# Performance work log

Measured on AMD Instinct MI355X. Metric: run time of the kernel, lower is better.

Reference implementation:

```python
import jax, jax.numpy as jnp
from jax import lax
import numpy as np

# Mamba2 config from PixelMamba.__init__
D_MODEL = 128; D_STATE = 256; D_CONV = 4; EXPAND = 4; HEADDIM = 32
D_INNER = EXPAND * D_MODEL              # 512
NHEADS = D_INNER // HEADDIM             # 16
NGROUPS = 1
D_XBC = D_INNER + 2 * NGROUPS * D_STATE # 1024 (conv channels)
D_IN_PROJ = 2 * D_INNER + 2 * NGROUPS * D_STATE + NHEADS  # 1552
CHUNK = 128                             # SSD chunk length


def setup_inputs() -> dict:
    key = jax.random.key(0)
    ks = jax.random.split(key, 10)
    Bb, C, H, W = 2, 3, 64, 64
    f32 = jnp.float32
    rn = lambda k, shape, s: jax.random.normal(k, shape, f32) * s
    return {
        "x": jax.random.normal(ks[0], (Bb, C, H, W), f32),
        "fc0_w": rn(ks[1], (3, D_MODEL), 1.0 / np.sqrt(3.0)),
        "fc0_b": rn(ks[2], (D_MODEL,), 0.01),
        "in_proj_w": rn(ks[3], (D_MODEL, D_IN_PROJ), 1.0 / np.sqrt(D_MODEL)),
        "conv_w": rn(ks[4], (D_XBC, D_CONV), 1.0 / np.sqrt(D_CONV)),
        "conv_b": rn(ks[5], (D_XBC,), 0.01),
        "dt_bias": jnp.log(jnp.expm1(jax.random.uniform(ks[6], (NHEADS,), f32, 0.001, 0.1))),
        "A_log": jnp.log(jax.random.uniform(ks[7], (NHEADS,), f32, 1.0, 16.0)),
        "D": rn(ks[8], (NHEADS,), 1.0),
        "norm_w": jnp.ones((D_INNER,), f32),
        "out_proj_w": rn(ks[9], (D_INNER, D_MODEL), 1.0 / np.sqrt(D_INNER)),
    }


def _mamba2(u, in_proj_w, conv_w, conv_b, dt_bias, A_log, D, norm_w, out_proj_w):
    # u: (B, L, d_model)
    Bb, L, _ = u.shape
    zxbcdt = u @ in_proj_w                                     # (B,L,1552)
    z = zxbcdt[..., :D_INNER]                                  # gate
    xBC = zxbcdt[..., D_INNER:D_INNER + D_XBC]
    dt = jax.nn.softplus(zxbcdt[..., -NHEADS:] + dt_bias)     # (B,L,H)

    # causal depthwise conv1d + SiLU
    xc = lax.conv_general_dilated(
        xBC.transpose(0, 2, 1), conv_w[:, None, :], (1,), [(D_CONV - 1, 0)],
        dimension_numbers=('NCH', 'OIH', 'NCH'), feature_group_count=D_XBC)
    xBC = jax.nn.silu(xc + conv_b[None, :, None]).transpose(0, 2, 1)

    xs = xBC[..., :D_INNER].reshape(Bb, L, NHEADS, HEADDIM)    # (B,L,H,P)
    Bm = xBC[..., D_INNER:D_INNER + D_STATE]                   # (B,L,N), ngroups=1
    Cm = xBC[..., D_INNER + D_STATE:]                          # (B,L,N)
    A = -jnp.exp(A_log)                                        # (H,) negative

    # ---- SSD chunked selective scan ----
    NC = L // CHUNK
    a = (dt * A).reshape(Bb, NC, CHUNK, NHEADS)                # log-decay per step (<=0)
    dt_r = dt.reshape(Bb, NC, CHUNK, NHEADS)
    x_r = xs.reshape(Bb, NC, CHUNK, NHEADS, HEADDIM)
    B_r = Bm.reshape(Bb, NC, CHUNK, D_STATE)
    C_r = Cm.reshape(Bb, NC, CHUNK, D_STATE)
    cum = jnp.cumsum(a, axis=2)                                # (B,NC,Q,H)

    # intra-chunk quadratic part: attn[t,s] = (C_t.B_s) * exp(cum_t - cum_s) * dt_s, s<=t
    mask = jnp.tril(jnp.ones((CHUNK, CHUNK), bool))
    diff = cum[:, :, :, None, :] - cum[:, :, None, :, :]       # (B,NC,t,s,H)
    decay = jnp.exp(jnp.where(mask[None, None, :, :, None], diff, -jnp.inf))
    CB = jnp.einsum('bctn,bcsn->bcts', C_r, B_r)
    attn = CB[..., None] * decay * dt_r[:, :, None, :, :]      # (B,NC,t,s,H)
    y_intra = jnp.einsum('bctsh,bcshp->bcthp', attn, x_r)

    # per-chunk end states: sum_s exp(cum_end - cum_s) dt_s x_s B_s^T
    decay_end = jnp.exp(cum[:, :, -1:, :] - cum)               # (B,NC,Q,H)
    states = jnp.einsum('bcsh,bcsn,bcshp->bchpn', decay_end * dt_r, B_r, x_r)

    # inter-chunk recurrence over NC chunks (small sequential scan)
    chunk_decay = jnp.exp(cum[:, :, -1, :])                    # (B,NC,H)
    def step(S, inp):
        cd, st = inp
        return S * cd[..., None, None] + st, S                 # emit state BEFORE chunk
    S0 = jnp.zeros((Bb, NHEADS, HEADDIM, D_STATE), u.dtype)
    _, prev = lax.scan(step, S0, (chunk_decay.transpose(1, 0, 2),
                                  states.transpose(1, 0, 2, 3, 4)))
    prev = prev.transpose(1, 0, 2, 3, 4)                       # (B,NC,H,P,N)
    y_inter = jnp.einsum('bcth,bctn,bchpn->bcthp', jnp.exp(cum), C_r, prev)

    y = (y_intra + y_inter).reshape(Bb, L, NHEADS, HEADDIM) + D[None, None, :, None] * xs
    y = y.reshape(Bb, L, D_INNER)

    # gated RMSNorm (norm_before_gate=False): norm(y * silu(z)) * w
    y = y * jax.nn.silu(z)
    y = y * lax.rsqrt(jnp.mean(y * y, axis=-1, keepdims=True) + 1e-5) * norm_w
    return y @ out_proj_w


def reference(x, fc0_w, fc0_b, in_proj_w, conv_w, conv_b, dt_bias, A_log, D, norm_w, out_proj_w):
    Bb, C, H, W = x.shape
    x1 = x.transpose(0, 2, 3, 1).reshape(Bb, -1, C)            # raster order
    x2 = x[:, :, ::-1, ::-1].transpose(0, 2, 3, 1).reshape(Bb, -1, C)  # flipped
    u = jnp.concatenate([x1, x2], axis=1) @ fc0_w + fc0_b      # (B, 2HW, 128)
    return _mamba2(u, in_proj_w, conv_w, conv_b, dt_bias, A_log, D, norm_w, out_proj_w)
```

## Files before the change

### kernel.cpp

```cpp
#include <hip/hip_runtime.h>
#include <hip/hip_bf16.h>

typedef short short8 __attribute__((ext_vector_type(8)));
typedef float f32x4 __attribute__((ext_vector_type(4)));
typedef unsigned short ushort;
typedef unsigned int uint;

#define MFMA16(a,b,c) __builtin_amdgcn_mfma_f32_16x16x32_bf16(a,b,c,0,0,0)
#define DPROJ 1552
#define LOG2E 1.44269504f

constexpr size_t OFF_M    = 0;
constexpr size_t OFF_CB_B = 0x5000;
constexpr size_t OFF_WT   = 0x8000;
constexpr size_t OFF_XT   = 0x30000;
constexpr size_t OFF_DT   = OFF_XT  + 16777216ull;
constexpr size_t OFF_BCM  = OFF_DT  + 1048576ull;
constexpr size_t OFF_CUM  = OFF_BCM + 16777216ull;
constexpr size_t OFF_CDC  = OFF_CUM + 1048576ull;
constexpr size_t OFF_CBT  = OFF_CDC + 8192ull;
constexpr size_t OFF_BT   = OFF_CBT + 4194304ull;
constexpr size_t OFF_ST   = OFF_BT  + 8388608ull;
constexpr size_t OFF_Y    = OFF_ST  + 33554432ull;

__device__ __forceinline__ float sigm(float x){ return 1.0f/(1.0f + __expf(-x)); }
__device__ __forceinline__ ushort f2bf(float f){
  union { __hip_bfloat16 h; ushort u; } c;
  c.h = __float2bfloat16(f);
  return c.u;
}
__device__ __forceinline__ float bf2f(ushort h){
  union { uint u; float f; } c; c.u = ((uint)h)<<16;
  return c.f;
}
__device__ __forceinline__ void swz2048(int p, int& bc, int& h){
  int xcd = p & 7, slot = p >> 3;
  bc = xcd*16 + (slot >> 4);
  h  = slot & 15;
}

__global__ __launch_bounds__(256) void k0m_prep(const float* __restrict__ fc0_w,
                                                const float* __restrict__ fc0_b,
                                                const float* __restrict__ W,
                                                const float* __restrict__ norm_w,
                                                const float* __restrict__ Wout,
                                                char* __restrict__ wsb){
  int d = blockIdx.x;
  ushort* WT = (ushort*)(wsb + OFF_WT);
  for (int i = threadIdx.x; i < 512; i += 256)
    WT[(size_t)d*512 + i] = f2bf(norm_w[i]*Wout[(size_t)i*128 + d]);
  if (d < 7){
    int j = d*256 + threadIdx.x;
    if (j >= DPROJ) return;
    float* Mo = (float*)(wsb + OFF_M);
    float* Co = (float*)(wsb + OFF_CB_B);
    float m0=0.f,m1=0.f,m2=0.f,cc=0.f;
    for (int dd=0; dd<128; ++dd){
      float w = W[(size_t)dd*DPROJ + j];
      m0 = fmaf(fc0_w[dd],     w, m0);
      m1 = fmaf(fc0_w[128+dd], w, m1);
      m2 = fmaf(fc0_w[256+dd], w, m2);
      cc = fmaf(fc0_b[dd],     w, cc);
    }
    Mo[j] = m0; Mo[DPROJ + j] = m1; Mo[2*DPROJ + j] = m2;
    Co[j] = cc;
  }
}

__device__ __forceinline__ void proj8(int li, const float* __restrict__ xb,
                                      const float* m0, const float* m1, const float* m2,
                                      const float* c8, float* dst){
  if (li < 0){
    #pragma unroll
    for (int j=0;j<8;++j) dst[j] = 0.f;
    return;
  }
  int hh, wv;
  if (li < 4096){ hh = li>>6; wv = li&63; }
  else { int l2 = li-4096; hh = 63-(l2>>6); wv = 63-(l2&63); }
  float x0 = xb[hh*64+wv], x1 = xb[4096+hh*64+wv], x2 = xb[8192+hh*64+wv];
  #pragma unroll
  for (int j=0;j<8;++j)
    dst[j] = fmaf(x2, m2[j], fmaf(x1, m1[j], fmaf(x0, m0[j], c8[j])));
}

__device__ __forceinline__ void conv8(const float* cb8, const float* cw0, const float* cw1,
                                      const float* cw2, const float* cw3,
                                      const float* wA, const float* wB,
                                      const float* wC, const float* wD, ushort* o){
  #pragma unroll
  for (int j=0;j<8;++j){
    float a = cb8[j];
    a = fmaf(wA[j], cw0[j], a);
    a = fmaf(wB[j], cw1[j], a);
    a = fmaf(wC[j], cw2[j], a);
    a = fmaf(wD[j], cw3[j], a);
    o[j] = f2bf(a * sigm(a));
  }
}

__global__ __launch_bounds__(256) void k12_projconv(const float* __restrict__ x,
                                                    const float* __restrict__ conv_w,
                                                    const float* __restrict__ conv_b,
                                                    char* __restrict__ wsb){
  int tid = threadIdx.x;
  int cg = tid & 127, rl = tid >> 7;
  int row0 = blockIdx.x*16 + rl*8;
  int b = row0 >> 13, l0 = row0 & 8191;
  const float* M  = (const float*)(wsb + OFF_M);
  const float* Cc = (const float*)(wsb + OFF_CB_B);
  const float* xb = x + (size_t)b*12288;
  int ch0 = cg*8, j0 = 512 + ch0;
  float m0[8],m1[8],m2[8],c8[8],cw0[8],cw1[8],cw2[8],cw3[8],cb8[8];
  #pragma unroll
  for (int j=0;j<8;++j){
    m0[j]=M[j0+j]; m1[j]=M[DPROJ+j0+j]; m2[j]=M[2*DPROJ+j0+j]; c8[j]=Cc[j0+j];
    cw0[j]=conv_w[(ch0+j)*4+0]; cw1[j]=conv_w[(ch0+j)*4+1];
    cw2[j]=conv_w[(ch0+j)*4+2]; cw3[j]=conv_w[(ch0+j)*4+3];
    cb8[j]=conv_b[ch0+j];
  }
  bool is_xs = (ch0 < 512);
  bool is_b  = (ch0 >= 512) && (ch0 < 768);
  bool pack  = is_xs || is_b;
  ushort* bcmp = (ushort*)(wsb + OFF_BCM);
  int chb = ch0 - 512;
  uint colw[8][4];
  ushort oprev[8];
  float w0[8],w1[8],w2[8],w3[8];
  ushort o[8];
  proj8(l0-3, xb, m0,m1,m2,c8, w1);
  proj8(l0-2, xb, m0,m1,m2,c8, w2);
  proj8(l0-1, xb, m0,m1,m2,c8, w3);

#define ROW_EVEN(R, WN, WA, WB, WC)                                          \
  proj8(l0+R, xb, m0,m1,m2,c8, WN);                                          \
  conv8(cb8,cw0,cw1,cw2,cw3, WA,WB,WC,WN, o);                                \
  if (pack){ _Pragma("unroll")                                               \
    for (int j=0;j<8;++j) oprev[j] = o[j]; }                                 \
  if (!is_xs) *(uint4*)(bcmp + (size_t)(row0+R)*512 + chb) = *(uint4*)o;
#define ROW_ODD(R, WN, WA, WB, WC)                                           \
  proj8(l0+R, xb, m0,m1,m2,c8, WN);                                          \
  conv8(cb8,cw0,cw1,cw2,cw3, WA,WB,WC,WN, o);                                \
  if (pack){ _Pragma("unroll")                                               \
    for (int j=0;j<8;++j) colw[j][(R)>>1] = (uint)oprev[j] | ((uint)o[j]<<16); } \
  if (!is_xs) *(uint4*)(bcmp + (size_t)(row0+R)*512 + chb) = *(uint4*)o;

  ROW_EVEN(0, w0, w1,w2,w3)
  ROW_ODD (1, w1, w2,w3,w0)
  ROW_EVEN(2, w2, w3,w0,w1)
  ROW_ODD (3, w3, w0,w1,w2)
  ROW_EVEN(4, w0, w1,w2,w3)
  ROW_ODD (5, w1, w2,w3,w0)
  ROW_EVEN(6, w2, w3,w0,w1)
  ROW_ODD (7, w3, w0,w1,w2)
#undef ROW_EVEN
#undef ROW_ODD

  int bc = row0>>7, grp = (row0&127)>>3;
  if (is_xs){
    int h = ch0>>5, p0 = ch0&31;
    ushort* dst = (ushort*)(wsb+OFF_XT) + (((size_t)(bc*16+h)*16 + grp)*32)*8;
    #pragma unroll
    for (int j=0;j<8;++j){
      uint4 v; v.x = colw[j][0]; v.y = colw[j][1]; v.z = colw[j][2]; v.w = colw[j][3];
      *(uint4*)(dst + (size_t)(p0+j)*8) = v;
    }
  } else if (is_b){
    ushort* btb = (ushort*)(wsb+OFF_BT) + (size_t)bc*32768;
    #pragma unroll
    for (int j=0;j<8;++j){
      uint4 v; v.x = colw[j][0]; v.y = colw[j][1]; v.z = colw[j][2]; v.w = colw[j][3];
      *(uint4*)(btb + (size_t)(grp*256 + chb + j)*8) = v;
    }
  }
}

__global__ __launch_bounds__(256) void k4m(const float* __restrict__ x,
                                           const float* __restrict__ dt_bias,
                                           const float* __restrict__ A_log,
                                           char* __restrict__ wsb){
  __shared__ __align__(16) char sMem[20480];
  int tid = threadIdx.x;
  int lane = tid&63, wid = tid>>6, l15 = lane&15, l4 = lane>>4;

  if (blockIdx.x < 2048){
    int bc, h; swz2048(blockIdx.x, bc, h);
    int bi = bc*16 + h;
    float* sCS = (float*)sMem;
    float* sW  = (float*)(sMem + 512);
    const ushort* xt  = (const ushort*)(wsb + OFF_XT) + (size_t)bi*4096;
    const ushort* btb = (const ushort*)(wsb + OFF_BT) + (size_t)bc*32768;
    ushort* st = (ushort*)(wsb + OFF_ST) + (size_t)bi*8192;
    float dtv = 0.f;
    if (tid < 128){
      int r = bc*128 + tid;
      int b = r >> 13, l = r & 8191;
      int hp, wv;
      if (l < 4096){ hp = l>>6; wv = l&63; }
      else { int l2 = l-4096; hp = 63-(l2>>6); wv = 63-(l2&63); }
      const float* xb = x + (size_t)b*12288;
      float x0 = xb[hp*64+wv], x1 = xb[4096+hp*64+wv], x2 = xb[8192+hp*64+wv];
      const float* M  = (const float*)(wsb + OFF_M);
      const float* Cc = (const float*)(wsb + OFF_CB_B);
      int j = 1536 + h;
      float v = Cc[j];
      v = fmaf(x0, M[j], v);
      v = fmaf(x1, M[DPROJ+j], v);
      v = fmaf(x2, M[2*DPROJ+j], v);
      float tt = v + dt_bias[h];
      dtv = (tt > 20.f) ? tt : log1pf(__expf(tt));
      ((float*)(wsb+OFF_DT))[(size_t)r*16 + h] = dtv;
      float A2 = -__expf(A_log[h]) * LOG2E;
      sCS[tid] = dtv * A2;
    }
    __syncthreads();
    for (int off=1; off<128; off<<=1){
      float sv = (tid>=off && tid<128) ? sCS[tid-off] : 0.f;
      __syncthreads();
      if (tid < 128) sCS[tid] += sv;
      __syncthreads();
    }
    if (tid < 128){
      float cv = sCS[tid];
      ((float*)(wsb + OFF_CUM))[(size_t)bi*128 + tid] = cv;
      if (tid == 127) ((float*)(wsb + OFF_CDC))[bi] = exp2f(cv);
    }
    __syncthreads();
    if (tid < 128) sW[tid] = exp2f(sCS[127] - sCS[tid]) * dtv;
    __syncthreads();
    f32x4 acc2[2][4] = {};
    #pragma unroll
    for (int ks = 0; ks < 4; ++ks){
      int grp = ks*4 + l4;
      const float* wp = sW + grp*8;
      short8 ra0 = *(const short8*)(xt + (size_t)(grp*32 + l15)*8);
      short8 ra1 = *(const short8*)(xt + (size_t)(grp*32 + 16 + l15)*8);
      short8 a0, a1;
      #pragma unroll
      for (int j=0;j<8;++j){
        a0[j] = (short)f2bf(bf2f((ushort)ra0[j]) * wp[j]);
        a1[j] = (short)f2bf(bf2f((ushort)ra1[j]) * wp[j]);
      }
      #pragma unroll
      for (int ntl = 0; ntl < 4; ++ntl){
        int n = wid*64 + ntl*16 + l15;
        short8 b = *(const short8*)(btb + (size_t)(grp*256 + n)*8);
        acc2[0][ntl] = MFMA16(a0,b,acc2[0][ntl]);
        acc2[1][ntl] = MFMA16(a1,b,acc2[1][ntl]);
      }
    }
    #pragma unroll
    for (int mt=0; mt<2; ++mt)
    #pragma unroll
    for (int ntl=0; ntl<4; ++ntl)
    #pragma unroll
    for (int r=0; r<4; ++r){
      int p = mt*16 + l4*4 + r;
      int n = wid*64 + ntl*16 + l15;
      st[(size_t)((n>>3)*32 + p)*8 + (n&7)] = f2bf(acc2[mt][ntl][r]);
    }
  } else {
    int bi = blockIdx.x - 2048;
    int sq = bi & 3; int bc = bi >> 2;
    char* sC = sMem;
    char* sB = sMem + 16384;
    const ushort* bcm = (const ushort*)(wsb + OFF_BCM);
    ushort* cbtT = (ushort*)(wsb + OFF_CBT) + (size_t)bc*16384;
    size_t rb = (size_t)bc*128;
    int s_base = sq*32;
    f32x4 acc[2][2] = {};
    for (int nt = 0; nt < 4; ++nt){
      int n0 = nt*64;
      __syncthreads();
      for (int idx = tid; idx < 1024; idx += 256){
        int t = idx>>3, c = idx&7;
        uint4 v = *(const uint4*)(bcm + (rb+t)*512 + 256 + n0 + c*8);
        *(uint4*)(sC + ((t*128 + c*16) ^ ((t&7)<<4))) = v;
      }
      {
        int idx = tid;
        int s = idx>>3, c = idx&7;
        uint4 v = *(const uint4*)(bcm + (rb+s_base+s)*512 + n0 + c*8);
        *(uint4*)(sB + ((s*128 + c*16) ^ ((s&7)<<4))) = v;
      }
      __syncthreads();
      if (wid >= sq){
        #pragma unroll
        for (int ks = 0; ks < 2; ++ks){
          int kb = ks*64 + l4*16;
          int t0 = wid*32 + l15, t1 = t0 + 16;
          short8 a0 = *(const short8*)(sC + ((t0*128 + kb) ^ ((t0&7)<<4)));
          short8 a1 = *(const short8*)(sC + ((t1*128 + kb) ^ ((t1&7)<<4)));
          short8 b0 = *(const short8*)(sB + ((l15*128 + kb) ^ ((l15&7)<<4)));
          short8 b1 = *(const short8*)(sB + (((16+l15)*128 + kb) ^ (((16+l15)&7)<<4)));
          acc[0][0] = MFMA16(a0,b0,acc[0][0]);
          acc[0][1] = MFMA16(a0,b1,acc[0][1]);
          acc[1][0] = MFMA16(a1,b0,acc[1][0]);
          acc[1][1] = MFMA16(a1,b1,acc[1][1]);
        }
      }
    }
    #pragma unroll
    for (int mt=0; mt<2; ++mt)
    #pragma unroll
    for (int st=0; st<2; ++st)
    #pragma unroll
    for (int r=0; r<4; ++r){
      int t = wid*32 + mt*16 + l4*4 + r;
      int s = s_base + st*16 + l15;
      float v = (t >= s) ? acc[mt][st][r] : 0.f;
      cbtT[(size_t)((s>>3)*128 + t)*8 + (s&7)] = f2bf(v);
    }
  }
}

__global__ __launch_bounds__(256) void k5_scan(char* __restrict__ wsb){
  int g = blockIdx.x*256 + threadIdx.x;
  int idx32 = g*2;
  int e = idx32 & 7;
  int q = idx32 >> 3;
  int p = q & 31; q >>= 5;
  int grp = q & 31; q >>= 5;
  int h = q & 15; int b = q >> 4;
  int off32 = (grp*32 + p)*4 + (e>>1);
  uint* st32 = (uint*)(wsb + OFF_ST);
  const float* cdc = (const float*)(wsb + OFF_CDC);
  float S0 = 0.f, S1 = 0.f;
  for (int c=0; c<64; ++c){
    int bi = (b*64+c)*16 + h;
    size_t idx = (size_t)bi*4096 + off32;
    uint v = st32[idx];
    float v0 = bf2f((ushort)(v & 0xFFFFu));
    float v1 = bf2f((ushort)(v >> 16));
    st32[idx] = (uint)f2bf(S0) | ((uint)f2bf(S1) << 16);
    float cd = cdc[bi];
    S0 = fmaf(S0, cd, v0);
    S1 = fmaf(S1, cd, v1);
  }
}

__global__ __launch_bounds__(256) void k4y_out(const float* __restrict__ Dp,
                                               char* __restrict__ wsb){
  int bc, h; swz2048(blockIdx.x, bc, h);
  int bi = bc*16 + h;
  __shared__ float sCum[128], sDt[128], sE[128];
  __shared__ __align__(16) char sPrev[16384];
  __shared__ __align__(16) char sXT[8192];
  const ushort* cbt = (const ushort*)(wsb + OFF_CBT) + (size_t)bc*16384;
  const char* xtg   = (const char*)(wsb + OFF_XT) + (size_t)bi*8192;
  const char* prevg = (const char*)(wsb + OFF_ST) + (size_t)bi*16384;
  const ushort* bcm = (const ushort*)(wsb + OFF_BCM);
  const float* cum  = (const float*)(wsb + OFF_CUM) + (size_t)bi*128;
  const float* dtp  = (const float*)(wsb + OFF_DT);
  ushort* Yb = (ushort*)(wsb + OFF_Y);
  size_t rb = (size_t)bc*128;
  int tid = threadIdx.x;
  #pragma unroll
  for (int i=0;i<4;++i)
    *(uint4*)(sPrev + i*4096 + tid*16) = *(const uint4*)(prevg + (size_t)i*4096 + tid*16);
  #pragma unroll
  for (int i=0;i<2;++i)
    *(uint4*)(sXT + i*4096 + tid*16) = *(const uint4*)(xtg + (size_t)i*4096 + tid*16);
  if (tid < 128){
    float cv = cum[tid];
    sCum[tid] = cv;
    sDt[tid]  = dtp[(rb+tid)*16 + h];
    sE[tid]   = exp2f(cv);
  }
  __syncthreads();
  int lane = tid&63, wid = tid>>6, l15 = lane&15, l4 = lane>>4;
  int t0 = wid*32 + l15, t1 = t0 + 16;
  float ct0 = sCum[t0], ct1 = sCum[t1];
  f32x4 acc[2][2] = {};
  #pragma unroll
  for (int ks = 0; ks < 4; ++ks){
    if (ks <= wid){
      int grp = ks*4 + l4;
      int s0 = grp*8;
      short8 ra0 = *(const short8*)(cbt + (size_t)(grp*128 + t0)*8);
      short8 ra1 = *(const short8*)(cbt + (size_t)(grp*128 + t1)*8);
      short8 a0, a1;
      #pragma unroll
      for (int j=0;j<8;++j){
        int s = s0 + j;
        float cs = sCum[s], ds = sDt[s];
        float e0 = exp2f(fminf(ct0 - cs, 0.f)) * ds;
        float e1 = exp2f(fminf(ct1 - cs, 0.f)) * ds;
        a0[j] = (short)f2bf(bf2f((ushort)ra0[j]) * e0);
        a1[j] = (short)f2bf(bf2f((ushort)ra1[j]) * e1);
      }
      short8 b0 = *(const short8*)(sXT + (grp*32 + l15)*16);
      short8 b1 = *(const short8*)(sXT + (grp*32 + 16 + l15)*16);
      acc[0][0] = MFMA16(a0,b0,acc[0][0]);
      acc[0][1] = MFMA16(a0,b1,acc[0][1]);
      acc[1][0] = MFMA16(a1,b0,acc[1][0]);
      acc[1][1] = MFMA16(a1,b1,acc[1][1]);
    }
  }
  f32x4 acc2[2][2] = {};
  #pragma unroll
  for (int ks = 0; ks < 8; ++ks){
    int koff = ks*32 + l4*8;
    int grp = ks*4 + l4;
    short8 a0 = *(const short8*)(bcm + (rb+t0)*512 + 256 + koff);
    short8 a1 = *(const short8*)(bcm + (rb+t1)*512 + 256 + koff);
    short8 b0 = *(const short8*)(sPrev + (grp*32 + l15)*16);
    short8 b1 = *(const short8*)(sPrev + (grp*32 + 16 + l15)*16);
    acc2[0][0] = MFMA16(a0,b0,acc2[0][0]);
    acc2[0][1] = MFMA16(a0,b1,acc2[0][1]);
    acc2[1][0] = MFMA16(a1,b0,acc2[1][0]);
    acc2[1][1] = MFMA16(a1,b1,acc2[1][1]);
  }
  float Dh = Dp[h];
  #pragma unroll
  for (int mt=0; mt<2; ++mt){
    int tb = wid*32 + mt*16 + l4*4;
    int tg = tb>>3, e0i = tb&7;
    #pragma unroll
    for (int nt=0; nt<2; ++nt){
      int p = nt*16 + l15;
      ushort xv[4];
      *(uint2*)xv = *(const uint2*)(sXT + ((tg*32 + p)*8 + e0i)*2);
      #pragma unroll
      for (int r=0; r<4; ++r){
        int t = tb + r;
        float yv = acc[mt][nt][r] + sE[t]*acc2[mt][nt][r] + Dh*bf2f(xv[r]);
        Yb[(rb+t)*512 + h*32 + p] = f2bf(yv);
      }
    }
  }
}

__global__ __launch_bounds__(256) void k7_final(const float* __restrict__ x,
                                                char* __restrict__ wsb,
                                                float* __restrict__ out){
  int r0 = blockIdx.x*32;
  __shared__ __align__(16) char sG[32768];
  __shared__ float sScale[32];
  const ushort* Yb = (const ushort*)(wsb + OFF_Y);
  const float* M  = (const float*)(wsb + OFF_M);
  const float* Cb = (const float*)(wsb + OFF_CB_B);
  const ushort* WT = (const ushort*)(wsb + OFF_WT);
  int tid = threadIdx.x;
  int r = tid>>3, li = tid&7;
  int row = r0 + r; int b = row>>13, l = row & 8191;
  int hh, wv;
  if (l < 4096){ hh = l>>6; wv = l&63; }
  else { int l2 = l-4096; hh = 63-(l2>>6); wv = 63-(l2&63); }
  const float* xb = x + (size_t)b*12288;
  float x0 = xb[hh*64+wv], x1 = xb[4096+hh*64+wv], x2 = xb[8192+hh*64+wv];
  float sq = 0.f;
  #pragma unroll
  for (int k = 0; k < 8; ++k){
    int i0 = li*64 + k*8;
    short8 yv = *(const short8*)(Yb + (size_t)row*512 + i0);
    ushort g8[8];
    #pragma unroll
    for (int j=0;j<8;++j){
      int i = i0 + j;
      float z = Cb[i];
      z = fmaf(x0, M[i], z);
      z = fmaf(x1, M[DPROJ+i], z);
      z = fmaf(x2, M[2*DPROJ+i], z);
      float g = bf2f((ushort)yv[j]) * z * sigm(z);
      sq = fmaf(g, g, sq);
      g8[j] = f2bf(g);
    }
    *(uint4*)(sG + ((r*1024 + i0*2) ^ ((r&7)<<4))) = *(uint4*)g8;
  }
  sq += __shfl_xor(sq, 1, 64);
  sq += __shfl_xor(sq, 2, 64);
  sq += __shfl_xor(sq, 4, 64);
  if (li == 0) sScale[r] = rsqrtf(sq*(1.f/512.f) + 1e-5f);
  __syncthreads();
  int lane = tid&63, wid = tid>>6, l15 = lane&15, l4 = lane>>4;
  f32x4 acc[2][2] = {};
  #pragma unroll
  for (int ks = 0; ks < 16; ++ks){
    int kb = ks*64 + l4*16;
    int rr0 = l15, rr1 = 16+l15;
    short8 a0 = *(const short8*)(sG + ((rr0*1024 + kb) ^ ((rr0&7)<<4)));
    short8 a1 = *(const short8*)(sG + ((rr1*1024 + kb) ^ ((rr1&7)<<4)));
    int koff = ks*32 + l4*8;
    short8 b0 = *(const short8*)(WT + (size_t)(wid*32 + l15)*512 + koff);
    short8 b1 = *(const short8*)(WT + (size_t)(wid*32 + 16 + l15)*512 + koff);
    acc[0][0] = MFMA16(a0,b0,acc[0][0]);
    acc[0][1] = MFMA16(a0,b1,acc[0][1]);
    acc[1][0] = MFMA16(a1,b0,acc[1][0]);
    acc[1][1] = MFMA16(a1,b1,acc[1][1]);
  }
  #pragma unroll
  for (int mt=0; mt<2; ++mt)
  #pragma unroll
  for (int nt=0; nt<2; ++nt)
  #pragma unroll
  for (int r4=0; r4<4; ++r4){
    int rr = mt*16 + l4*4 + r4;
    int d = wid*32 + nt*16 + l15;
    out[(size_t)(r0+rr)*128 + d] = acc[mt][nt][r4] * sScale[rr];
  }
}

extern "C" void kernel_launch(void* const* d_in, const int* in_sizes, int n_in,
                              void* d_out, int out_size, void* d_ws, size_t ws_size,
                              hipStream_t stream) {
  const float* x         = (const float*)d_in[0];
  const float* fc0_w     = (const float*)d_in[1];
  const float* fc0_b     = (const float*)d_in[2];
  const float* in_proj_w = (const float*)d_in[3];
  const float* conv_w    = (const float*)d_in[4];
  const float* conv_b    = (const float*)d_in[5];
  const float* dt_bias   = (const float*)d_in[6];
  const float* A_log     = (const float*)d_in[7];
  const float* Dp        = (const float*)d_in[8];
  const float* norm_w    = (const float*)d_in[9];
  const float* out_proj_w= (const float*)d_in[10];
  char* wsb  = (char*)d_ws;
  float* out = (float*)d_out;

  k0m_prep<<<dim3(128),  dim3(256), 0, stream>>>(fc0_w, fc0_b, in_proj_w, norm_w, out_proj_w, wsb);
  k12_projconv<<<dim3(1024), dim3(256), 0, stream>>>(x, conv_w, conv_b, wsb);
  k4m    <<<dim3(2560),  dim3(256), 0, stream>>>(x, dt_bias, A_log, wsb);
  k5_scan<<<dim3(512),   dim3(256), 0, stream>>>(wsb);
  k4y_out<<<dim3(2048),  dim3(256), 0, stream>>>(Dp, wsb);
  k7_final<<<dim3(512),  dim3(256), 0, stream>>>(x, wsb, out);
}
```

Baseline: 138.4 us.

## Rework k4m: wave-shuffle cumsum, direct-global CB GEMM, reorder block roles

The 128-element cumulative sum of dt*A is now done with wavefront shuffle-up scans plus one shared-memory fixup, replacing the barrier-heavy log-step scan. The C·B^T block branch now reads operands straight from global memory instead of staging them through swizzled LDS tiles, and the full K=256 loop runs without barriers. The CB blocks are moved to the front of the grid, and shared memory shrinks to two small float arrays, which should raise occupancy. The cost is more uncached or uncoalesced global reads of the B/C rows in the CB branch.

Result: no change. 137.8 us (median of 2 runs) (-0.4%).

```diff
diff --git a/kernel.cpp b/kernel.cpp
--- a/kernel.cpp
+++ b/kernel.cpp
@@ -179,125 +179,32 @@
                                            const float* __restrict__ dt_bias,
                                            const float* __restrict__ A_log,
                                            char* __restrict__ wsb){
-  __shared__ __align__(16) char sMem[20480];
+  __shared__ float sCS[128];
+  __shared__ float sW[128];
   int tid = threadIdx.x;
   int lane = tid&63, wid = tid>>6, l15 = lane&15, l4 = lane>>4;
 
-  if (blockIdx.x < 2048){
-    int bc, h; swz2048(blockIdx.x, bc, h);
-    int bi = bc*16 + h;
-    float* sCS = (float*)sMem;
-    float* sW  = (float*)(sMem + 512);
-    const ushort* xt  = (const ushort*)(wsb + OFF_XT) + (size_t)bi*4096;
-    const ushort* btb = (const ushort*)(wsb + OFF_BT) + (size_t)bc*32768;
-    ushort* st = (ushort*)(wsb + OFF_ST) + (size_t)bi*8192;
-    float dtv = 0.f;
-    if (tid < 128){
-      int r = bc*128 + tid;
-      int b = r >> 13, l = r & 8191;
-      int hp, wv;
-      if (l < 4096){ hp = l>>6; wv = l&63; }
-      else { int l2 = l-4096; hp = 63-(l2>>6); wv = 63-(l2&63); }
-      const float* xb = x + (size_t)b*12288;
-      float x0 = xb[hp*64+wv], x1 = xb[4096+hp*64+wv], x2 = xb[8192+hp*64+wv];
-      const float* M  = (const float*)(wsb + OFF_M);
-      const float* Cc = (const float*)(wsb + OFF_CB_B);
-      int j = 1536 + h;
-      float v = Cc[j];
-      v = fmaf(x0, M[j], v);
-      v = fmaf(x1, M[DPROJ+j], v);
-      v = fmaf(x2, M[2*DPROJ+j], v);
-      float tt = v + dt_bias[h];
-      dtv = (tt > 20.f) ? tt : log1pf(__expf(tt));
-      ((float*)(wsb+OFF_DT))[(size_t)r*16 + h] = dtv;
-      float A2 = -__expf(A_log[h]) * LOG2E;
-      sCS[tid] = dtv * A2;
-    }
-    __syncthreads();
-    for (int off=1; off<128; off<<=1){
-      float sv = (tid>=off && tid<128) ? sCS[tid-off] : 0.f;
-      __syncthreads();
-      if (tid < 128) sCS[tid] += sv;
-      __syncthreads();
-    }
-    if (tid < 128){
-      float cv = sCS[tid];
-      ((float*)(wsb + OFF_CUM))[(size_t)bi*128 + tid] = cv;
-      if (tid == 127) ((float*)(wsb + OFF_CDC))[bi] = exp2f(cv);
-    }
-    __syncthreads();
-    if (tid < 128) sW[tid] = exp2f(sCS[127] - sCS[tid]) * dtv;
-    __syncthreads();
-    f32x4 acc2[2][4] = {};
-    #pragma unroll
-    for (int ks = 0; ks < 4; ++ks){
-      int grp = ks*4 + l4;
-      const float* wp = sW + grp*8;
-      short8 ra0 = *(const short8*)(xt + (size_t)(grp*32 + l15)*8);
-      short8 ra1 = *(const short8*)(xt + (size_t)(grp*32 + 16 + l15)*8);
-      short8 a0, a1;
-      #pragma unroll
-      for (int j=0;j<8;++j){
-        a0[j] = (short)f2bf(bf2f((ushort)ra0[j]) * wp[j]);
-        a1[j] = (short)f2bf(bf2f((ushort)ra1[j]) * wp[j]);
-      }
-      #pragma unroll
-      for (int ntl = 0; ntl < 4; ++ntl){
-        int n = wid*64 + ntl*16 + l15;
-        short8 b = *(const short8*)(btb + (size_t)(grp*256 + n)*8);
-        acc2[0][ntl] = MFMA16(a0,b,acc2[0][ntl]);
-        acc2[1][ntl] = MFMA16(a1,b,acc2[1][ntl]);
-      }
-    }
-    #pragma unroll
-    for (int mt=0; mt<2; ++mt)
-    #pragma unroll
-    for (int ntl=0; ntl<4; ++ntl)
-    #pragma unroll
-    for (int r=0; r<4; ++r){
-      int p = mt*16 + l4*4 + r;
-      int n = wid*64 + ntl*16 + l15;
-      st[(size_t)((n>>3)*32 + p)*8 + (n&7)] = f2bf(acc2[mt][ntl][r]);
-    }
-  } else {
-    int bi = blockIdx.x - 2048;
-    int sq = bi & 3; int bc = bi >> 2;
-    char* sC = sMem;
-    char* sB = sMem + 16384;
+  if (blockIdx.x < 512){
+    int bi4 = blockIdx.x;
+    int sq = bi4 & 3; int bc = bi4 >> 2;
     const ushort* bcm = (const ushort*)(wsb + OFF_BCM);
     ushort* cbtT = (ushort*)(wsb + OFF_CBT) + (size_t)bc*16384;
     size_t rb = (size_t)bc*128;
     int s_base = sq*32;
     f32x4 acc[2][2] = {};
-    for (int nt = 0; nt < 4; ++nt){
-      int n0 = nt*64;
-      __syncthreads();
-      for (int idx = tid; idx < 1024; idx += 256){
-        int t = idx>>3, c = idx&7;
-        uint4 v = *(const uint4*)(bcm + (rb+t)*512 + 256 + n0 + c*8);
-        *(uint4*)(sC + ((t*128 + c*16) ^ ((t&7)<<4))) = v;
-      }
-      {
-        int idx = tid;
-        int s = idx>>3, c = idx&7;
-        uint4 v = *(const uint4*)(bcm + (rb+s_base+s)*512 + n0 + c*8);
-        *(uint4*)(sB + ((s*128 + c*16) ^ ((s&7)<<4))) = v;
-      }
-      __syncthreads();
-      if (wid >= sq){
-        #pragma unroll
-        for (int ks = 0; ks < 2; ++ks){
-          int kb = ks*64 + l4*16;
-          int t0 = wid*32 + l15, t1 = t0 + 16;
-          short8 a0 = *(const short8*)(sC + ((t0*128 + kb) ^ ((t0&7)<<4)));
-          short8 a1 = *(const short8*)(sC + ((t1*128 + kb) ^ ((t1&7)<<4)));
-          short8 b0 = *(const short8*)(sB + ((l15*128 + kb) ^ ((l15&7)<<4)));
-          short8 b1 = *(const short8*)(sB + (((16+l15)*128 + kb) ^ (((16+l15)&7)<<4)));
-          acc[0][0] = MFMA16(a0,b0,acc[0][0]);
-          acc[0][1] = MFMA16(a0,b1,acc[0][1]);
-          acc[1][0] = MFMA16(a1,b0,acc[1][0]);
-          acc[1][1] = MFMA16(a1,b1,acc[1][1]);
-        }
+    if (wid >= sq){
+      int t0 = wid*32 + l15, t1 = t0 + 16;
+      #pragma unroll
+      for (int kk = 0; kk < 8; ++kk){
+        int ko = kk*32 + l4*8;
+        short8 a0 = *(const short8*)(bcm + (rb+t0)*512 + 256 + ko);
+        short8 a1 = *(const short8*)(bcm + (rb+t1)*512 + 256 + ko);
+        short8 b0 = *(const short8*)(bcm + (rb + s_base + l15)*512 + ko);
+        short8 b1 = *(const short8*)(bcm + (rb + s_base + 16 + l15)*512 + ko);
+        acc[0][0] = MFMA16(a0,b0,acc[0][0]);
+        acc[0][1] = MFMA16(a0,b1,acc[0][1]);
+        acc[1][0] = MFMA16(a1,b0,acc[1][0]);
+        acc[1][1] = MFMA16(a1,b1,acc[1][1]);
       }
     }
     #pragma unroll
@@ -311,6 +218,82 @@
       float v = (t >= s) ? acc[mt][st][r] : 0.f;
       cbtT[(size_t)((s>>3)*128 + t)*8 + (s&7)] = f2bf(v);
     }
+    return;
+  }
+
+  int bc, h; swz2048(blockIdx.x - 512, bc, h);
+  int bi = bc*16 + h;
+  const ushort* xt  = (const ushort*)(wsb + OFF_XT) + (size_t)bi*4096;
+  const ushort* btb = (const ushort*)(wsb + OFF_BT) + (size_t)bc*32768;
+  ushort* st = (ushort*)(wsb + OFF_ST) + (size_t)bi*8192;
+  float dtv = 0.f, v = 0.f;
+  if (tid < 128){
+    int r = bc*128 + tid;
+    int b = r >> 13, l = r & 8191;
+    int hp, wv;
+    if (l < 4096){ hp = l>>6; wv = l&63; }
+    else { int l2 = l-4096; hp = 63-(l2>>6); wv = 63-(l2&63); }
+    const float* xb = x + (size_t)b*12288;
+    float x0 = xb[hp*64+wv], x1 = xb[4096+hp*64+wv], x2 = xb[8192+hp*64+wv];
+    const float* M  = (const float*)(wsb + OFF_M);
+    const float* Cc = (const float*)(wsb + OFF_CB_B);
+    int j = 1536 + h;
+    float vv = Cc[j];
+    vv = fmaf(x0, M[j], vv);
+    vv = fmaf(x1, M[DPROJ+j], vv);
+    vv = fmaf(x2, M[2*DPROJ+j], vv);
+    float tt = vv + dt_bias[h];
+    dtv = (tt > 20.f) ? tt : log1pf(__expf(tt));
+    ((float*)(wsb+OFF_DT))[(size_t)r*16 + h] = dtv;
+    float A2 = -__expf(A_log[h]) * LOG2E;
+    v = dtv * A2;
+  }
+  #pragma unroll
+  for (int off=1; off<64; off<<=1){
+    float u = __shfl_up(v, off, 64);
+    if (lane >= off) v += u;
+  }
+  if (tid < 128) sCS[tid] = v;
+  __syncthreads();
+  if (tid >= 64 && tid < 128) sCS[tid] = v + sCS[63];
+  __syncthreads();
+  if (tid < 128){
+    float cv = sCS[tid];
+    ((float*)(wsb + OFF_CUM))[(size_t)bi*128 + tid] = cv;
+    if (tid == 127) ((float*)(wsb + OFF_CDC))[bi] = exp2f(cv);
+    sW[tid] = exp2f(sCS[127] - cv) * dtv;
+  }
+  __syncthreads();
+  f32x4 acc2[2][4] = {};
+  #pragma unroll
+  for (int ks = 0; ks < 4; ++ks){
+    int grp = ks*4 + l4;
+    const float* wp = sW + grp*8;
+    short8 ra0 = *(const short8*)(xt + (size_t)(grp*32 + l15)*8);
+    short8 ra1 = *(const short8*)(xt + (size_t)(grp*32 + 16 + l15)*8);
+    short8 a0, a1;
+    #pragma unroll
+    for (int j=0;j<8;++j){
+      a0[j] = (short)f2bf(bf2f((ushort)ra0[j]) * wp[j]);
+      a1[j] = (short)f2bf(bf2f((ushort)ra1[j]) * wp[j]);
+    }
+    #pragma unroll
+    for (int ntl = 0; ntl < 4; ++ntl){
+      int n = wid*64 + ntl*16 + l15;
+      short8 b = *(const short8*)(btb + (size_t)(grp*256 + n)*8);
+      acc2[0][ntl] = MFMA16(a0,b,acc2[0][ntl]);
+      acc2[1][ntl] = MFMA16(a1,b,acc2[1][ntl]);
+    }
+  }
+  #pragma unroll
+  for (int mt=0; mt<2; ++mt)
+  #pragma unroll
+  for (int ntl=0; ntl<4; ++ntl)
+  #pragma unroll
+  for (int r=0; r<4; ++r){
+    int p = mt*16 + l4*4 + r;
+    int n = wid*64 + ntl*16 + l15;
+    st[(size_t)((n>>3)*32 + p)*8 + (n&7)] = f2bf(acc2[mt][ntl][r]);
   }
 }
 
```
